# Optimization experiments

Hardware: AMD Instinct MI355X
Metric: run time of the kernel (lower is better)

Reference implementation:

```python
import jax, jax.numpy as jnp
import numpy as np

L = 10.0
N_UP = 2048
N_DN = 2048
N = N_UP + N_DN
HIDDEN = 32


def _neural_decayed(x, w1, b1, wo, bo):
    # x: (M,) pair distances. Tiny MLP 1 -> HIDDEN -> 1 with compact-support decay.
    x_cut = L / 2
    xn = jnp.clip(x / x_cut, 0.0, 1.0 - 1e-05)
    decay = jnp.exp(1.0 - 1.0 / (1.0 - xn ** 2))
    h = jax.nn.swish(decay[:, None] @ w1 + b1)      # (M, HIDDEN)
    out = (h @ wo + bo).ravel()                      # (M,)
    return out * decay


def setup_inputs() -> dict:
    key = jax.random.key(0)
    ks = jax.random.split(key, 9)
    rs = jax.random.uniform(ks[0], (N, 3), dtype=jnp.float32) * L
    s = 1.0 / np.sqrt(HIDDEN)
    return {
        "rs": rs,
        "same_w1": jax.random.normal(ks[1], (1, HIDDEN), jnp.float32),
        "same_b1": jnp.zeros((HIDDEN,), jnp.float32),
        "same_wo": jax.random.normal(ks[2], (HIDDEN, 1), jnp.float32) * s,
        "same_bo": jnp.zeros((1,), jnp.float32),
        "diff_w1": jax.random.normal(ks[3], (1, HIDDEN), jnp.float32),
        "diff_b1": jnp.zeros((HIDDEN,), jnp.float32),
        "diff_wo": jax.random.normal(ks[4], (HIDDEN, 1), jnp.float32) * s,
        "diff_bo": jnp.zeros((1,), jnp.float32),
    }


def reference(rs, same_w1, same_b1, same_wo, same_bo, diff_w1, diff_b1, diff_wo, diff_bo):
    # Pairwise minimum-image displacements: (N, N, 3)
    disps = rs[:, None, :] - rs[None, :, :]
    disps = (disps + L / 2) % L - L / 2
    mask = ~jnp.eye(N, dtype=bool)
    disps = jnp.where(mask[:, :, None], disps, 0.0)
    r_ij = jnp.sqrt(jnp.sum(disps ** 2, axis=-1) + 1e-15)  # (N, N)

    up_up = r_ij[:N_UP, :N_UP]
    dn_dn = r_ij[N_UP:, N_UP:]
    up_dn = r_ij[N_UP:, :N_UP]

    f_uu = _neural_decayed(up_up.ravel(), same_w1, same_b1, same_wo, same_bo).reshape(up_up.shape)
    f_dd = _neural_decayed(dn_dn.ravel(), same_w1, same_b1, same_wo, same_bo).reshape(dn_dn.shape)
    f_ud = _neural_decayed(up_dn.ravel(), diff_w1, diff_b1, diff_wo, diff_bo).reshape(up_dn.shape)

    forces = jnp.zeros((N, N), jnp.float32)
    forces = forces.at[:N_UP, :N_UP].set(f_uu)
    forces = forces.at[N_UP:, N_UP:].set(f_dd)
    forces = forces.at[N_UP:, :N_UP].set(f_ud)
    forces = forces.at[:N_UP, N_UP:].set(f_ud.T)
    forces = jnp.where(mask, forces, 0.0)

    backflow = jnp.sum(forces[:, :, None] * disps, axis=1)  # (N, 3)
    return rs + backflow
```

## Files before the change

### kernel.cpp

```cpp
#include <hip/hip_runtime.h>

#define N_TOT 4096
#define N_UPC 2048
#define HID 32
#define M_LUT 2048
#define ITILE 256
#define JCH 64

__device__ float2 g_lut[2 * M_LUT];

__device__ __forceinline__ float eval_F(float s, const float* __restrict__ w1,
                                        const float* __restrict__ b1,
                                        const float* __restrict__ wo, float bo) {
  float r = sqrtf(s + 1e-15f);
  float xn = fminf(r * 0.2f, 1.0f - 1e-5f);
  float dcy = __expf(1.0f - 1.0f / (1.0f - xn * xn));
  float acc = bo;
#pragma unroll
  for (int k = 0; k < HID; ++k) {
    float z = fmaf(dcy, w1[k], b1[k]);
    float h = z / (1.0f + __expf(-z));
    acc = fmaf(h, wo[k], acc);
  }
  return acc * dcy;
}

__global__ void lut_init_kernel(const float* __restrict__ rs,
    const float* __restrict__ sw1, const float* __restrict__ sb1,
    const float* __restrict__ swo, const float* __restrict__ sbo,
    const float* __restrict__ dw1, const float* __restrict__ db1,
    const float* __restrict__ dwo, const float* __restrict__ dbo,
    float* __restrict__ out) {
  const float DSF = 25.0f / (float)(M_LUT - 1);
  int t = blockIdx.x * blockDim.x + threadIdx.x;
  if (t < 2 * M_LUT) {
    int tab = t >> 11;
    int m = t & (M_LUT - 1);
    const float* w1 = tab ? dw1 : sw1;
    const float* b1 = tab ? db1 : sb1;
    const float* wo = tab ? dwo : swo;
    float bo = tab ? dbo[0] : sbo[0];
    float s0 = m * DSF;
    float f0 = eval_F(s0, w1, b1, wo, bo);
    float f1 = eval_F(s0 + DSF, w1, b1, wo, bo);
    g_lut[t] = make_float2(f0, f1 - f0);
  }
  if (t < 3 * N_TOT) out[t] = rs[t];
}

__global__ __launch_bounds__(256) void pair_kernel(const float* __restrict__ rs,
                                                   float* __restrict__ out) {
  __shared__ float2 lut[2 * M_LUT];
  for (int t = threadIdx.x; t < 2 * M_LUT; t += ITILE) lut[t] = g_lut[t];

  int itile = blockIdx.x & 15;
  int jc = blockIdx.x >> 4;
  int i = itile * ITILE + threadIdx.x;
  float xi = rs[3 * i + 0];
  float yi = rs[3 * i + 1];
  float zi = rs[3 * i + 2];
  __syncthreads();

  const bool same_spin = ((jc < (N_UPC / JCH)) == (itile < 8));
  const float2* __restrict__ tab = lut + (same_spin ? 0 : M_LUT);
  const float INV_DS = (float)(M_LUT - 1) / 25.0f;
  const float UMAX = (float)(M_LUT - 1);

  float ax = 0.f, ay = 0.f, az = 0.f;
  int j0 = jc * JCH;
#pragma unroll 8
  for (int jj = 0; jj < JCH; ++jj) {
    int j = j0 + jj;
    float dx = xi - rs[3 * j + 0];
    float dy = yi - rs[3 * j + 1];
    float dz = zi - rs[3 * j + 2];
    dx = fmaf(-10.0f, rintf(dx * 0.1f), dx);
    dy = fmaf(-10.0f, rintf(dy * 0.1f), dy);
    dz = fmaf(-10.0f, rintf(dz * 0.1f), dz);
    float s = fmaf(dx, dx, fmaf(dy, dy, dz * dz));
    float u = fminf(s * INV_DS, UMAX);
    int idx = (int)u;
    float w = u - (float)idx;
    float2 e = tab[idx];
    float F = fmaf(w, e.y, e.x);
    ax = fmaf(F, dx, ax);
    ay = fmaf(F, dy, ay);
    az = fmaf(F, dz, az);
  }
  atomicAdd(&out[3 * i + 0], ax);
  atomicAdd(&out[3 * i + 1], ay);
  atomicAdd(&out[3 * i + 2], az);
}

extern "C" void kernel_launch(void* const* d_in, const int* in_sizes, int n_in,
                              void* d_out, int out_size, void* d_ws, size_t ws_size,
                              hipStream_t stream) {
  const float* rs = (const float*)d_in[0];
  lut_init_kernel<<<64, 256, 0, stream>>>(
      rs,
      (const float*)d_in[1], (const float*)d_in[2], (const float*)d_in[3],
      (const float*)d_in[4],
      (const float*)d_in[5], (const float*)d_in[6], (const float*)d_in[7],
      (const float*)d_in[8],
      (float*)d_out);
  pair_kernel<<<(N_TOT / ITILE) * (N_TOT / JCH), ITILE, 0, stream>>>(
      rs, (float*)d_out);
}
```

Before: 90.63 us.

## Replace shared-memory LUT with Chebyshev polynomial fit of MLP in decay variable

The per-pair 2048-entry interpolated lookup table in shared memory is replaced by a degree-15 polynomial in the decay value. The init kernel fits the MLP with Chebyshev nodes and converts the result to monomial coefficients, which are held in registers. The pair kernel then computes rcp, exp and a 15-step Horner evaluation per pair instead of doing a shared-memory gather. This removes the LUT staging and LDS bank conflicts but adds about 17 FMAs plus transcendentals per pair, and converting to the monomial basis may lose accuracy.

```diff
diff --git a/kernel.cpp b/kernel.cpp
--- a/kernel.cpp
+++ b/kernel.cpp
@@ -1,74 +1,105 @@
 #include <hip/hip_runtime.h>
+#include <math.h>
 
 #define N_TOT 4096
 #define N_UPC 2048
 #define HID 32
-#define M_LUT 2048
+#define NC 16
 #define ITILE 256
 #define JCH 64
 
-__device__ float2 g_lut[2 * M_LUT];
+__device__ float g_coef[2][NC];
 
-__device__ __forceinline__ float eval_F(float s, const float* __restrict__ w1,
-                                        const float* __restrict__ b1,
-                                        const float* __restrict__ wo, float bo) {
-  float r = sqrtf(s + 1e-15f);
-  float xn = fminf(r * 0.2f, 1.0f - 1e-5f);
-  float dcy = __expf(1.0f - 1.0f / (1.0f - xn * xn));
-  float acc = bo;
-#pragma unroll
-  for (int k = 0; k < HID; ++k) {
-    float z = fmaf(dcy, w1[k], b1[k]);
-    float h = z / (1.0f + __expf(-z));
-    acc = fmaf(h, wo[k], acc);
-  }
-  return acc * dcy;
-}
-
-__global__ void lut_init_kernel(const float* __restrict__ rs,
+__global__ void fit_init_kernel(const float* __restrict__ rs,
     const float* __restrict__ sw1, const float* __restrict__ sb1,
     const float* __restrict__ swo, const float* __restrict__ sbo,
     const float* __restrict__ dw1, const float* __restrict__ db1,
     const float* __restrict__ dwo, const float* __restrict__ dbo,
     float* __restrict__ out) {
-  const float DSF = 25.0f / (float)(M_LUT - 1);
-  int t = blockIdx.x * blockDim.x + threadIdx.x;
-  if (t < 2 * M_LUT) {
-    int tab = t >> 11;
-    int m = t & (M_LUT - 1);
+  int gtid = blockIdx.x * blockDim.x + threadIdx.x;
+  if (gtid < 3 * N_TOT) out[gtid] = rs[gtid];
+  if (blockIdx.x != 0) return;
+
+  const int tid = threadIdx.x;
+  const float PI = 3.14159265358979323846f;
+  __shared__ float Gv[2][NC];
+  __shared__ float cb[2][NC];
+  __shared__ float Tm2[NC], Tm1[NC], mono0[NC], mono1[NC];
+
+  if (tid < 2 * NC) {
+    int tab = tid >> 4, m = tid & (NC - 1);
     const float* w1 = tab ? dw1 : sw1;
     const float* b1 = tab ? db1 : sb1;
     const float* wo = tab ? dwo : swo;
     float bo = tab ? dbo[0] : sbo[0];
-    float s0 = m * DSF;
-    float f0 = eval_F(s0, w1, b1, wo, bo);
-    float f1 = eval_F(s0 + DSF, w1, b1, wo, bo);
-    g_lut[t] = make_float2(f0, f1 - f0);
+    float um = cosf(PI * (m + 0.5f) / NC);
+    float t = 0.5f * (um + 1.0f);
+    float g = bo;
+    for (int k = 0; k < HID; ++k) {
+      float z = fmaf(t, w1[k], b1[k]);
+      g = fmaf(z / (1.0f + expf(-z)), wo[k], g);
+    }
+    Gv[tab][m] = g;
   }
-  if (t < 3 * N_TOT) out[t] = rs[t];
+  __syncthreads();
+
+  if (tid < 2 * NC) {
+    int tab = tid >> 4, j = tid & (NC - 1);
+    float c = 0.0f;
+    for (int m = 0; m < NC; ++m)
+      c += Gv[tab][m] * cosf(PI * j * (m + 0.5f) / NC);
+    c *= 2.0f / NC;
+    if (j == 0) c *= 0.5f;
+    cb[tab][j] = c;
+  }
+  __syncthreads();
+
+  if (tid < NC) {
+    Tm2[tid] = (tid == 0) ? 1.0f : 0.0f;
+    Tm1[tid] = (tid == 1) ? 1.0f : 0.0f;
+    mono0[tid] = cb[0][0] * Tm2[tid] + cb[0][1] * Tm1[tid];
+    mono1[tid] = cb[1][0] * Tm2[tid] + cb[1][1] * Tm1[tid];
+  }
+  __syncthreads();
+  for (int n = 2; n < NC; ++n) {
+    float tn = 0.0f;
+    if (tid < NC) {
+      float tkm1 = (tid >= 1) ? Tm1[tid - 1] : 0.0f;
+      tn = 2.0f * tkm1 - Tm2[tid];
+    }
+    __syncthreads();
+    if (tid < NC) {
+      Tm2[tid] = Tm1[tid];
+      Tm1[tid] = tn;
+      mono0[tid] = fmaf(cb[0][n], tn, mono0[tid]);
+      mono1[tid] = fmaf(cb[1][n], tn, mono1[tid]);
+    }
+    __syncthreads();
+  }
+  if (tid < NC) {
+    g_coef[0][tid] = mono0[tid];
+    g_coef[1][tid] = mono1[tid];
+  }
 }
 
 __global__ __launch_bounds__(256) void pair_kernel(const float* __restrict__ rs,
                                                    float* __restrict__ out) {
-  __shared__ float2 lut[2 * M_LUT];
-  for (int t = threadIdx.x; t < 2 * M_LUT; t += ITILE) lut[t] = g_lut[t];
-
   int itile = blockIdx.x & 15;
   int jc = blockIdx.x >> 4;
   int i = itile * ITILE + threadIdx.x;
   float xi = rs[3 * i + 0];
   float yi = rs[3 * i + 1];
   float zi = rs[3 * i + 2];
-  __syncthreads();
 
   const bool same_spin = ((jc < (N_UPC / JCH)) == (itile < 8));
-  const float2* __restrict__ tab = lut + (same_spin ? 0 : M_LUT);
-  const float INV_DS = (float)(M_LUT - 1) / 25.0f;
-  const float UMAX = (float)(M_LUT - 1);
+  const float* __restrict__ cfp = g_coef[same_spin ? 0 : 1];
+  float cf[NC];
+#pragma unroll
+  for (int k = 0; k < NC; ++k) cf[k] = cfp[k];
 
   float ax = 0.f, ay = 0.f, az = 0.f;
   int j0 = jc * JCH;
-#pragma unroll 8
+#pragma unroll 4
   for (int jj = 0; jj < JCH; ++jj) {
     int j = j0 + jj;
     float dx = xi - rs[3 * j + 0];
@@ -78,11 +109,14 @@
     dy = fmaf(-10.0f, rintf(dy * 0.1f), dy);
     dz = fmaf(-10.0f, rintf(dz * 0.1f), dz);
     float s = fmaf(dx, dx, fmaf(dy, dy, dz * dz));
-    float u = fminf(s * INV_DS, UMAX);
-    int idx = (int)u;
-    float w = u - (float)idx;
-    float2 e = tab[idx];
-    float F = fmaf(w, e.y, e.x);
+    float u = fminf(s * 0.04f, 0.99998f);
+    float r = __builtin_amdgcn_rcpf(1.0f - u);
+    float t = __expf(1.0f - r);
+    float w = fmaf(2.0f, t, -1.0f);
+    float P = cf[NC - 1];
+#pragma unroll
+    for (int k = NC - 2; k >= 0; --k) P = fmaf(P, w, cf[k]);
+    float F = t * P;
     ax = fmaf(F, dx, ax);
     ay = fmaf(F, dy, ay);
     az = fmaf(F, dz, az);
@@ -96,7 +130,7 @@
                               void* d_out, int out_size, void* d_ws, size_t ws_size,
                               hipStream_t stream) {
   const float* rs = (const float*)d_in[0];
-  lut_init_kernel<<<64, 256, 0, stream>>>(
+  fit_init_kernel<<<48, 256, 0, stream>>>(
       rs,
       (const float*)d_in[1], (const float*)d_in[2], (const float*)d_in[3],
       (const float*)d_in[4],
```

Result: slower. 98.40 us (+8.6%).
